# Optimization experiments

Measured on AMD Instinct MI355X. Metric: run time of the kernel, lower is better.

The kernel has to match this reference:

```python
import jax, jax.numpy as jnp
import numpy as np

T, N, E = 8, 50000, 800000
XD, HD, GD, ZD, TD, YHD = 128, 256, 128, 128, 8, 16
PSH = 100          # ps_predictor hidden width
BN_EPS = 1e-5


def _dense(k, fan_in, shape):
    return jax.random.normal(k, shape, jnp.float32) * (1.0 / np.sqrt(fan_in))


def setup_inputs() -> dict:
    ks = jax.random.split(jax.random.key(0), 20)
    inp = {}
    inp["X"] = jax.random.normal(ks[0], (T, N, XD), jnp.float32)
    inp["C"] = jax.random.uniform(ks[1], (T, N, TD), dtype=jnp.float32)
    inp["Y_hist"] = jax.random.normal(ks[2], (T, N, YHD), jnp.float32)
    inp["edge_index"] = jax.random.randint(ks[3], (T, 2, E), 0, N)
    # parameters
    inp["phi_W"] = _dense(ks[4], XD, (XD, HD)); inp["phi_b"] = jnp.zeros((HD,), jnp.float32)
    inp["gc_W"] = _dense(ks[5], HD, (T, HD, GD)); inp["gc_b"] = jnp.zeros((T, GD), jnp.float32)
    inp["ew_logit"] = jax.random.normal(ks[6], (T, E), jnp.float32) * 0.1  # learned edge weights (pre-sigmoid)
    inp["fuse_W"] = _dense(ks[7], 2 * HD + GD, (2 * HD + GD, ZD)); inp["fuse_b"] = jnp.zeros((ZD,), jnp.float32)
    inp["o00_W"] = _dense(ks[8], ZD, (ZD, ZD)); inp["o00_b"] = jnp.zeros((ZD,), jnp.float32)
    inp["o10_W"] = _dense(ks[9], ZD, (ZD, ZD)); inp["o10_b"] = jnp.zeros((ZD,), jnp.float32)
    inp["o01_W"] = _dense(ks[10], ZD, (ZD, 1)); inp["o01_b"] = jnp.zeros((1,), jnp.float32)
    inp["o11_W"] = _dense(ks[11], ZD, (ZD, 1)); inp["o11_b"] = jnp.zeros((1,), jnp.float32)
    inp["ps1_W"] = _dense(ks[12], ZD, (ZD, PSH)); inp["ps1_b"] = jnp.zeros((PSH,), jnp.float32)
    inp["bn_g"] = jnp.ones((PSH,), jnp.float32); inp["bn_b"] = jnp.zeros((PSH,), jnp.float32)
    inp["ps2_W"] = _dense(ks[13], PSH, (PSH, 2)); inp["ps2_b"] = jnp.zeros((2,), jnp.float32)
    inp["gru_Wih"] = _dense(ks[14], ZD + TD + YHD, (3 * HD, ZD + TD + YHD))
    inp["gru_Whh"] = _dense(ks[15], HD, (3 * HD, HD))
    inp["gru_bih"] = jnp.zeros((3 * HD,), jnp.float32)
    inp["gru_bhh"] = jnp.zeros((3 * HD,), jnp.float32)
    return inp


def reference(X, C, Y_hist, edge_index, phi_W, phi_b, gc_W, gc_b, ew_logit,
              fuse_W, fuse_b, o00_W, o00_b, o10_W, o10_b, o01_W, o01_b,
              o11_W, o11_b, ps1_W, ps1_b, bn_g, bn_b, ps2_W, ps2_b,
              gru_Wih, gru_Whh, gru_bih, gru_bhh):
    h0 = jnp.zeros((N, HD), X.dtype)
    bn_scale = bn_g / jnp.sqrt(1.0 + BN_EPS)  # eval-mode BN: running_mean=0, running_var=1

    def step(h, xs):
        x, ei, c, yh, W_t, b_t, ewl_t = xs
        phi = jax.nn.relu(x @ phi_W + phi_b)                              # [N,HD]
        # --- GCNConv with learned sigmoid edge weights + self loops ---
        src, dst = ei[0], ei[1]
        ew = jax.nn.sigmoid(ewl_t)                                        # [E]
        deg = jax.ops.segment_sum(ew, dst, num_segments=N) + 1.0          # +1 for self-loop weight
        dinv = jax.lax.rsqrt(deg)
        norm = dinv[src] * ew * dinv[dst]                                 # symmetric norm per edge
        xw = phi @ W_t                                                    # [N,GD]
        agg = jax.ops.segment_sum(norm[:, None] * xw[src], dst, num_segments=N)
        agg = agg + xw / deg[:, None] + b_t                               # self-loop contribution + bias
        rep = jax.nn.relu(agg)                                            # [N,GD] (dropout off in eval)
        # --- fuse with skip connection ---
        z = jax.nn.relu(jnp.concatenate([h, rep, phi], axis=1) @ fuse_W + fuse_b)  # [N,ZD]
        # --- GRUCell (torch gate order: reset, update, new) ---
        inp = jnp.concatenate([z, c, yh], axis=1)
        gi = inp @ gru_Wih.T + gru_bih
        gh = h @ gru_Whh.T + gru_bhh
        i_r, i_z, i_n = jnp.split(gi, 3, axis=1)
        h_r, h_z, h_n = jnp.split(gh, 3, axis=1)
        r = jax.nn.sigmoid(i_r + h_r)
        u = jax.nn.sigmoid(i_z + h_z)
        n = jnp.tanh(i_n + r * h_n)
        h_new = (1.0 - u) * n + u * h
        # --- outcome heads ---
        y0 = jax.nn.relu(z @ o00_W + o00_b) @ o01_W + o01_b               # [N,1]
        y1 = jax.nn.relu(z @ o10_W + o10_b) @ o11_W + o11_b               # [N,1]
        # --- propensity head (BatchNorm eval, sigmoid, softmax) ---
        s = jax.nn.sigmoid((z @ ps1_W + ps1_b) * bn_scale + bn_b)
        ps = jax.nn.softmax(s @ ps2_W + ps2_b, axis=1)                    # [N,2]
        return h_new, (y1, y0, z, ps)

    h_fin, (all_y1, all_y0, all_z, all_ps) = jax.lax.scan(
        step, h0, (X, edge_index, C, Y_hist, gc_W, gc_b, ew_logit))
    return all_y1, all_y0, all_z, all_ps, h_fin
```

## Files before the change

### kernel.cpp

```cpp
#include <hip/hip_runtime.h>
#include <math.h>

#define T_STEPS 8
#define NN 50000
#define EE 800000
#define TN (T_STEPS*NN)
#define TE (T_STEPS*EE)

typedef unsigned int uint;
typedef unsigned short ushort;
typedef unsigned long long u64;
typedef __attribute__((ext_vector_type(8))) short short8;
typedef __attribute__((ext_vector_type(4))) float f32x4;

__device__ __forceinline__ float sigf(float x){ return 1.0f/(1.0f+expf(-x)); }
__device__ __forceinline__ ushort f2b(float f){
  uint x = __float_as_uint(f);
  uint r = (x + 0x7fffu + ((x>>16)&1u)) >> 16;
  return (ushort)r;
}
__device__ __forceinline__ float b2f(ushort u){ return __uint_as_float(((uint)u)<<16); }

__device__ __forceinline__ void gload16(const ushort* g, ushort* l){
  __builtin_amdgcn_global_load_lds(
      (const __attribute__((address_space(1))) void*)g,
      (__attribute__((address_space(3))) void*)l, 16, 0, 0);
}

template<int ROWS>
__device__ __forceinline__ void stage_tile(const ushort* base, int ld, int rowclamp,
                                           ushort* lds, int lane, int wid){
  constexpr int ITERS = ROWS/32;
#pragma unroll
  for (int i=0;i<ITERS;i++){
    int lin = i*256 + wid*64 + lane;
    int row = lin>>3, s = lin&7;
    int gr = row; if (gr > rowclamp) gr = rowclamp;
    const ushort* gp = base + (size_t)gr*ld + ((s ^ (row&7))<<3);
    gload16(gp, lds + (size_t)(i*256 + wid*64)*8);
  }
}

__device__ __forceinline__ short8 fragld(const ushort* lds, int R, int kk, int lane){
  int slot = (kk*4 + (lane>>4)) ^ (R&7);
  return *(const short8*)&lds[R*64 + slot*8];
}

struct Seg { const ushort* p; int ld; long ts; int w; };

__global__ __launch_bounds__(256,2) void gemm_bf(
    Seg s0, Seg s1, Seg s2,
    const ushort* __restrict__ W, int K2, long Wts,
    const float* __restrict__ bias, int act,
    const ushort* __restrict__ addp, int ldad, long adts,
    float* __restrict__ C32, int ldc, long c32ts,
    ushort* __restrict__ C16, int ldb, long c16ts,
    int Nrow, int NOvalid)
{
  __shared__ __align__(16) ushort As[8192];
  __shared__ __align__(16) ushort Bs[8192];
  const int t    = blockIdx.z;
  const int tid  = threadIdx.x;
  const int lane = tid & 63;
  const int wid  = __builtin_amdgcn_readfirstlane(tid >> 6);
  const int brow = blockIdx.x*128;
  const int bcol = blockIdx.y*128;
  const int wr = wid>>1, wc = wid&1;

  f32x4 acc[4][4];
#pragma unroll
  for(int m=0;m<4;m++)
#pragma unroll
    for(int n=0;n<4;n++) acc[m][n] = (f32x4){0.f,0.f,0.f,0.f};

  const int nk = K2 >> 6;
  for (int kt=0; kt<nk; ++kt){
    int col0 = kt*64;
    const ushort* ab; int ald;
    if (col0 < s0.w){ ab = s0.p + (size_t)t*s0.ts + col0; ald = s0.ld; }
    else if (col0 < s0.w + s1.w){ ab = s1.p + (size_t)t*s1.ts + (col0 - s0.w); ald = s1.ld; }
    else { ab = s2.p + (size_t)t*s2.ts + (col0 - s0.w - s1.w); ald = s2.ld; }
    stage_tile<128>(ab + (size_t)brow*ald, ald, Nrow-1-brow, As, lane, wid);
    stage_tile<128>(W + (size_t)t*Wts + (size_t)bcol*K2 + col0, K2, 1<<30, Bs, lane, wid);
    __syncthreads();
#pragma unroll
    for (int kk=0;kk<2;kk++){
      short8 a[4], b[4];
#pragma unroll
      for (int m=0;m<4;m++) a[m] = fragld(As, wr*64 + m*16 + (lane&15), kk, lane);
#pragma unroll
      for (int n=0;n<4;n++) b[n] = fragld(Bs, wc*64 + n*16 + (lane&15), kk, lane);
#pragma unroll
      for (int m=0;m<4;m++)
#pragma unroll
        for (int n=0;n<4;n++)
          acc[m][n] = __builtin_amdgcn_mfma_f32_16x16x32_bf16(a[m], b[n], acc[m][n], 0,0,0);
    }
    __syncthreads();
  }
  const int rbase = brow + wr*64 + (lane>>4)*4;
  const int cbase = bcol + wc*64 + (lane&15);
#pragma unroll
  for (int m=0;m<4;m++){
#pragma unroll
    for (int q=0;q<4;q++){
      int r = rbase + m*16 + q;
      if (r >= Nrow) continue;
#pragma unroll
      for (int n=0;n<4;n++){
        int c = cbase + n*16;
        if (c >= NOvalid) continue;
        float v = acc[m][n][q];
        if (addp) v += b2f(addp[(size_t)t*adts + (size_t)r*ldad + c]);
        if (bias) v += bias[c];
        if (act==1) v = fmaxf(v, 0.f);
        if (C32) C32[(size_t)t*c32ts + (size_t)r*ldc + c] = v;
        if (C16) C16[(size_t)t*c16ts + (size_t)r*ldb + c] = f2b(v);
      }
    }
  }
}

__global__ __launch_bounds__(256,2) void gemm_gru(
    Seg s0, Seg s1, Seg s2,
    const ushort* __restrict__ W,
    const float* __restrict__ bg,
    const float* __restrict__ hin,
    float* __restrict__ hout, ushort* __restrict__ hbfo,
    int Nrow)
{
  __shared__ __align__(16) ushort As[8192];
  __shared__ __align__(16) ushort Bs[8192];
  const int tid  = threadIdx.x;
  const int lane = tid & 63;
  const int wid  = __builtin_amdgcn_readfirstlane(tid >> 6);
  const int brow = blockIdx.x*128;
  const int bcol = blockIdx.y*128;
  const int wr = wid>>1, wc = wid&1;
  const int K2 = 448;

  f32x4 acc[4][4];
#pragma unroll
  for(int m=0;m<4;m++)
#pragma unroll
    for(int n=0;n<4;n++) acc[m][n] = (f32x4){0.f,0.f,0.f,0.f};

  for (int kt=0; kt<7; ++kt){
    int col0 = kt*64;
    const ushort* ab; int ald;
    if (col0 < s0.w){ ab = s0.p + col0; ald = s0.ld; }
    else if (col0 < s0.w + s1.w){ ab = s1.p + (col0 - s0.w); ald = s1.ld; }
    else { ab = s2.p + (col0 - s0.w - s1.w); ald = s2.ld; }
    stage_tile<128>(ab + (size_t)brow*ald, ald, Nrow-1-brow, As, lane, wid);
    stage_tile<128>(W + (size_t)bcol*K2 + col0, K2, 1<<30, Bs, lane, wid);
    __syncthreads();
#pragma unroll
    for (int kk=0;kk<2;kk++){
      short8 a[4], b[4];
#pragma unroll
      for (int m=0;m<4;m++) a[m] = fragld(As, wr*64 + m*16 + (lane&15), kk, lane);
#pragma unroll
      for (int n=0;n<4;n++) b[n] = fragld(Bs, wc*64 + n*16 + (lane&15), kk, lane);
#pragma unroll
      for (int m=0;m<4;m++)
#pragma unroll
        for (int n=0;n<4;n++)
          acc[m][n] = __builtin_amdgcn_mfma_f32_16x16x32_bf16(a[m], b[n], acc[m][n], 0,0,0);
    }
    __syncthreads();
  }
  const int jj = lane&15;
  const int j  = blockIdx.y*32 + wc*16 + jj;
  const int rbase = brow + wr*64 + (lane>>4)*4;
  const int bcolw = bcol + wc*64;
  float bb[4];
#pragma unroll
  for (int n=0;n<4;n++) bb[n] = bg[bcolw + n*16 + jj];
#pragma unroll
  for (int m=0;m<4;m++){
#pragma unroll
    for (int q=0;q<4;q++){
      int r = rbase + m*16 + q;
      if (r >= Nrow) continue;
      float v0 = acc[m][0][q] + bb[0];
      float v1 = acc[m][1][q] + bb[1];
      float v2 = acc[m][2][q] + bb[2];
      float v3 = acc[m][3][q] + bb[3];
      float rg = sigf(v0), ug = sigf(v1);
      float ng = tanhf(v2 + rg*v3);
      float ho = hin[(size_t)r*256 + j];
      float hn = (1.f-ug)*ng + ug*ho;
      hout[(size_t)r*256 + j] = hn;
      hbfo[(size_t)r*256 + j] = f2b(hn);
    }
  }
}

__global__ __launch_bounds__(256,2) void heads_k(
    const ushort* __restrict__ Az, long Ats,
    const ushort* __restrict__ W,
    const float* __restrict__ o00b, const float* __restrict__ o10b,
    const float* __restrict__ w01, const float* __restrict__ b01,
    const float* __restrict__ w11, const float* __restrict__ b11,
    float* __restrict__ y0out, long y0ts,
    float* __restrict__ y1out, long y1ts, int Nrow)
{
  __shared__ __align__(16) ushort As[4096];
  __shared__ __align__(16) ushort Bs[16384];
  __shared__ float shy[4][64];
  const int t    = blockIdx.z;
  const int tid  = threadIdx.x;
  const int lane = tid & 63;
  const int wid  = __builtin_amdgcn_readfirstlane(tid >> 6);
  const int brow = blockIdx.x*64;
  const ushort* A = Az + (size_t)t*Ats;

  f32x4 acc[4][4];
#pragma unroll
  for(int m=0;m<4;m++)
#pragma unroll
    for(int n=0;n<4;n++) acc[m][n] = (f32x4){0.f,0.f,0.f,0.f};

  for (int kt=0; kt<2; ++kt){
    stage_tile<64>(A + (size_t)brow*128 + kt*64, 128, Nrow-1-brow, As, lane, wid);
    stage_tile<256>(W + kt*64, 128, 1<<30, Bs, lane, wid);
    __syncthreads();
#pragma unroll
    for (int kk=0;kk<2;kk++){
      short8 a[4], b[4];
#pragma unroll
      for (int m=0;m<4;m++) a[m] = fragld(As, m*16 + (lane&15), kk, lane);
#pragma unroll
      for (int n=0;n<4;n++) b[n] = fragld(Bs, wid*64 + n*16 + (lane&15), kk, lane);
#pragma unroll
      for (int m=0;m<4;m++)
#pragma unroll
        for (int n=0;n<4;n++)
          acc[m][n] = __builtin_amdgcn_mfma_f32_16x16x32_bf16(a[m], b[n], acc[m][n], 0,0,0);
    }
    __syncthreads();
  }
  float bb[4], ww[4];
#pragma unroll
  for (int n=0;n<4;n++){
    int c = wid*64 + n*16 + (lane&15);
    bb[n] = (c<128)? o00b[c] : o10b[c-128];
    ww[n] = (c<128)? w01[c]  : w11[c-128];
  }
#pragma unroll
  for (int m=0;m<4;m++){
#pragma unroll
    for (int q=0;q<4;q++){
      float p = 0.f;
#pragma unroll
      for (int n=0;n<4;n++) p += fmaxf(acc[m][n][q] + bb[n], 0.f) * ww[n];
#pragma unroll
      for (int o=1;o<16;o<<=1) p += __shfl_xor(p, o);
      if ((lane&15)==0) shy[wid][m*16 + (lane>>4)*4 + q] = p;
    }
  }
  __syncthreads();
  if (tid < 64){
    int r = brow + tid;
    if (r < Nrow){
      y0out[(size_t)t*y0ts + r] = shy[0][tid] + shy[1][tid] + b01[0];
      y1out[(size_t)t*y1ts + r] = shy[2][tid] + shy[3][tid] + b11[0];
    }
  }
}

__global__ __launch_bounds__(256,2) void ps_k(
    const ushort* __restrict__ Az, long Ats,
    const ushort* __restrict__ W,
    const float* __restrict__ psc, const float* __restrict__ psb,
    const float* __restrict__ W2, const float* __restrict__ b2,
    float* __restrict__ psout, long psts, int Nrow)
{
  __shared__ __align__(16) ushort As[8192];
  __shared__ __align__(16) ushort Bs[8192];
  __shared__ float sh0[2][128];
  __shared__ float sh1[2][128];
  const int t    = blockIdx.z;
  const int tid  = threadIdx.x;
  const int lane = tid & 63;
  const int wid  = __builtin_amdgcn_readfirstlane(tid >> 6);
  const int brow = blockIdx.x*128;
  const int wr = wid>>1, wc = wid&1;
  const ushort* A = Az + (size_t)t*Ats;

  f32x4 acc[4][4];
#pragma unroll
  for(int m=0;m<4;m++)
#pragma unroll
    for(int n=0;n<4;n++) acc[m][n] = (f32x4){0.f,0.f,0.f,0.f};

  for (int kt=0; kt<2; ++kt){
    stage_tile<128>(A + (size_t)brow*128 + kt*64, 128, Nrow-1-brow, As, lane, wid);
    stage_tile<128>(W + kt*64, 128, 1<<30, Bs, lane, wid);
    __syncthreads();
#pragma unroll
    for (int kk=0;kk<2;kk++){
      short8 a[4], b[4];
#pragma unroll
      for (int m=0;m<4;m++) a[m] = fragld(As, wr*64 + m*16 + (lane&15), kk, lane);
#pragma unroll
      for (int n=0;n<4;n++) b[n] = fragld(Bs, wc*64 + n*16 + (lane&15), kk, lane);
#pragma unroll
      for (int m=0;m<4;m++)
#pragma unroll
        for (int n=0;n<4;n++)
          acc[m][n] = __builtin_amdgcn_mfma_f32_16x16x32_bf16(a[m], b[n], acc[m][n], 0,0,0);
    }
    __syncthreads();
  }
  float sc[4], sb[4], w0_[4], w1_[4];
#pragma unroll
  for (int n=0;n<4;n++){
    int c = wc*64 + n*16 + (lane&15);
    bool ok = (c<100);
    sc[n] = ok? psc[c] : 0.f;
    sb[n] = ok? psb[c] : 0.f;
    w0_[n]= ok? W2[2*c] : 0.f;
    w1_[n]= ok? W2[2*c+1] : 0.f;
  }
#pragma unroll
  for (int m=0;m<4;m++){
#pragma unroll
    for (int q=0;q<4;q++){
      float a0=0.f, a1=0.f;
#pragma unroll
      for (int n=0;n<4;n++){
        float s = sigf(acc[m][n][q]*sc[n] + sb[n]);
        a0 += s*w0_[n]; a1 += s*w1_[n];
      }
#pragma unroll
      for (int o=1;o<16;o<<=1){ a0 += __shfl_xor(a0,o); a1 += __shfl_xor(a1,o); }
      if ((lane&15)==0){
        int rt = wr*64 + m*16 + (lane>>4)*4 + q;
        sh0[wc][rt] = a0; sh1[wc][rt] = a1;
      }
    }
  }
  __syncthreads();
  if (tid < 128){
    int r = brow + tid;
    if (r < Nrow){
      float l0 = sh0[0][tid]+sh0[1][tid]+b2[0];
      float l1 = sh1[0][tid]+sh1[1][tid]+b2[1];
      float mx = fmaxf(l0,l1);
      float e0 = expf(l0-mx), e1 = expf(l1-mx);
      float inv = 1.f/(e0+e1);
      psout[(size_t)t*psts + (size_t)r*2]   = e0*inv;
      psout[(size_t)t*psts + (size_t)r*2+1] = e1*inv;
    }
  }
}

__global__ void count_k(const int* __restrict__ ei, const float* __restrict__ ewl,
                        u64* __restrict__ degcnt)
{
  int idx = blockIdx.x*256 + threadIdx.x;
  if (idx >= TE) return;
  int t = idx / EE;
  int e = idx - t*EE;
  const int* dst = ei + (size_t)t*2*EE + EE;
  int d = dst[e];
  u64 v = (1ULL<<40) | (u64)(uint)(sigf(ewl[idx]) * 1048576.0f);
  atomicAdd((unsigned long long*)&degcnt[t*NN + d], (unsigned long long)v);
}

__global__ void dinv_k(const u64* __restrict__ degcnt, int* __restrict__ cnt,
                       float* __restrict__ dnv, float* __restrict__ invd){
  int idx = blockIdx.x*256+threadIdx.x;
  if (idx>=TN) return;
  u64 tot = degcnt[idx];
  int c = (int)(tot>>40);
  float S = (float)(tot & ((1ULL<<40)-1)) * (1.f/1048576.f);
  float dv = S + 1.f;
  cnt[idx] = c;
  dnv[idx]  = rsqrtf(dv);
  invd[idx] = 1.f/dv;
}

__global__ void scan1_k(const int* __restrict__ in, int* __restrict__ outv,
                        int* __restrict__ partials, int n)
{
  __shared__ int sh[256];
  int base = blockIdx.x*1024;
  int tid = threadIdx.x;
  int v[4]; int s=0;
#pragma unroll
  for (int i=0;i<4;i++){ int idx=base+tid*4+i; v[i] = (idx<n)? in[idx]:0; s+=v[i]; }
  sh[tid]=s; __syncthreads();
  for (int o=1;o<256;o<<=1){
    int t2 = (tid>=o)? sh[tid-o]:0;
    __syncthreads();
    sh[tid]+=t2;
    __syncthreads();
  }
  int excl = sh[tid]-s;
#pragma unroll
  for (int i=0;i<4;i++){ int idx=base+tid*4+i; if(idx<n) outv[idx]=excl; excl+=v[i]; }
  if (tid==255) partials[blockIdx.x]=sh[255];
}

__global__ void scan2_k(int* p, int np){
  __shared__ int sh[256];
  __shared__ int run;
  int tid=threadIdx.x;
  if(tid==0) run=0;
  __syncthreads();
  for(int base=0;base<np;base+=256){
    int v = (base+tid<np)? p[base+tid]:0;
    sh[tid]=v; __syncthreads();
    for(int o=1;o<256;o<<=1){
      int t2 = (tid>=o)? sh[tid-o]:0;
      __syncthreads();
      sh[tid]+=t2;
      __syncthreads();
    }
    int incl=sh[tid];
    int r0=run;
    __syncthreads();
    if(base+tid<np) p[base+tid]=r0+incl-v;
    __syncthreads();
    if(tid==0) run = r0 + sh[255];
    __syncthreads();
  }
}

__global__ void scan3_k(int* __restrict__ offs, const int* __restrict__ parts,
                        int* __restrict__ cur, int n){
  int idx = blockIdx.x*256+threadIdx.x;
  if (idx==0) offs[n] = TE;
  if (idx<n){ int v = offs[idx] + parts[idx>>10]; offs[idx]=v; cur[idx]=v; }
}

__global__ void fill_k(const int* __restrict__ ei, const float* __restrict__ ewl,
                       const float* __restrict__ dnv, int* __restrict__ cur,
                       uint* __restrict__ epack)
{
  int idx = blockIdx.x*256 + threadIdx.x;
  if (idx >= TE) return;
  int t = idx / EE;
  int e = idx - t*EE;
  const int* srcp = ei + (size_t)t*2*EE;
  const int* dstp = srcp + EE;
  int s=srcp[e], d=dstp[e];
  float nr = dnv[t*NN+s] * sigf(ewl[idx]) * dnv[t*NN+d];
  uint nq = (uint)(nr*65535.f + 0.5f);
  int pos = atomicAdd(&cur[t*NN+d], 1);
  epack[pos] = (uint)s | (nq<<16);
}

__global__ __launch_bounds__(256) void gather_k(const int* __restrict__ offs,
    const uint* __restrict__ epack,
    const ushort* __restrict__ xwb, const float* __restrict__ invd,
    const float* __restrict__ gcb, ushort* __restrict__ rep)
{
  int t    = blockIdx.z;
  int node = blockIdx.x*4 + (threadIdx.x>>6);
  int lane = threadIdx.x & 63;
  int half = lane>>5, ll = lane&31;
  if (node >= NN) return;
  const int* offs_t = offs + (size_t)t*NN;
  const ushort* xw_t = xwb + (size_t)t*NN*128;
  int o0 = offs_t[node], o1 = offs_t[node+1];
  float a0=0.f, a1=0.f, a2=0.f, a3=0.f;

  int j = o0 + half;
  for (; j+6 < o1; j += 8){
    uint e0 = epack[j],   e1 = epack[j+2];
    uint e2 = epack[j+4], e3 = epack[j+6];
    uint2 v0 = ((const uint2*)(xw_t + (size_t)(e0&0xffff)*128))[ll];
    uint2 v1 = ((const uint2*)(xw_t + (size_t)(e1&0xffff)*128))[ll];
    uint2 v2 = ((const uint2*)(xw_t + (size_t)(e2&0xffff)*128))[ll];
    uint2 v3 = ((const uint2*)(xw_t + (size_t)(e3&0xffff)*128))[ll];
    float n0 = (float)(e0>>16), n1 = (float)(e1>>16);
    float n2 = (float)(e2>>16), n3 = (float)(e3>>16);
    a0 = fmaf(n0, b2f((ushort)(v0.x&0xffff)), a0);
    a1 = fmaf(n0, b2f((ushort)(v0.x>>16)),   a1);
    a2 = fmaf(n0, b2f((ushort)(v0.y&0xffff)), a2);
    a3 = fmaf(n0, b2f((ushort)(v0.y>>16)),   a3);
    a0 = fmaf(n1, b2f((ushort)(v1.x&0xffff)), a0);
    a1 = fmaf(n1, b2f((ushort)(v1.x>>16)),   a1);
    a2 = fmaf(n1, b2f((ushort)(v1.y&0xffff)), a2);
    a3 = fmaf(n1, b2f((ushort)(v1.y>>16)),   a3);
    a0 = fmaf(n2, b2f((ushort)(v2.x&0xffff)), a0);
    a1 = fmaf(n2, b2f((ushort)(v2.x>>16)),   a1);
    a2 = fmaf(n2, b2f((ushort)(v2.y&0xffff)), a2);
    a3 = fmaf(n2, b2f((ushort)(v2.y>>16)),   a3);
    a0 = fmaf(n3, b2f((ushort)(v3.x&0xffff)), a0);
    a1 = fmaf(n3, b2f((ushort)(v3.x>>16)),   a1);
    a2 = fmaf(n3, b2f((ushort)(v3.y&0xffff)), a2);
    a3 = fmaf(n3, b2f((ushort)(v3.y>>16)),   a3);
  }
  for (; j < o1; j += 2){
    uint e0 = epack[j];
    uint2 v0 = ((const uint2*)(xw_t + (size_t)(e0&0xffff)*128))[ll];
    float n0 = (float)(e0>>16);
    a0 = fmaf(n0, b2f((ushort)(v0.x&0xffff)), a0);
    a1 = fmaf(n0, b2f((ushort)(v0.x>>16)),   a1);
    a2 = fmaf(n0, b2f((ushort)(v0.y&0xffff)), a2);
    a3 = fmaf(n0, b2f((ushort)(v0.y>>16)),   a3);
  }
  a0 += __shfl_xor(a0, 32);
  a1 += __shfl_xor(a1, 32);
  a2 += __shfl_xor(a2, 32);
  a3 += __shfl_xor(a3, 32);
  const float qs = 1.f/65535.f;
  a0 *= qs; a1 *= qs; a2 *= qs; a3 *= qs;
  float sl = invd[(size_t)t*NN + node];
  uint2 us = ((const uint2*)(xw_t + (size_t)node*128))[ll];
  float4 gb = ((const float4*)(gcb + (size_t)t*128))[ll];
  a0 = fmaf(sl, b2f((ushort)(us.x&0xffff)), a0) + gb.x;
  a1 = fmaf(sl, b2f((ushort)(us.x>>16)),   a1) + gb.y;
  a2 = fmaf(sl, b2f((ushort)(us.y&0xffff)), a2) + gb.z;
  a3 = fmaf(sl, b2f((ushort)(us.y>>16)),   a3) + gb.w;
  a0 = fmaxf(a0,0.f); a1 = fmaxf(a1,0.f);
  a2 = fmaxf(a2,0.f); a3 = fmaxf(a3,0.f);
  if (half==0){
    uint pk0 = (uint)f2b(a0) | ((uint)f2b(a1)<<16);
    uint pk1 = (uint)f2b(a2) | ((uint)f2b(a3)<<16);
    ((uint2*)(rep + ((size_t)t*NN + node)*128))[ll] = make_uint2(pk0, pk1);
  }
}

__global__ void convT_k(ushort* __restrict__ dst, const float* __restrict__ src,
                        int O, int Osrc, int K, int Kp)
{
  int idx = blockIdx.x*256 + threadIdx.x;
  if (idx >= O*Kp) return;
  dst += (size_t)blockIdx.y * O * Kp;
  src += (size_t)blockIdx.y * K * Osrc;
  int o = idx / Kp, k = idx - o*Kp;
  float v = (k<K && o<Osrc) ? src[(size_t)k*Osrc + o] : 0.f;
  dst[idx] = f2b(v);
}

__global__ void woc_k(ushort* __restrict__ dst, const float* __restrict__ o00W,
                      const float* __restrict__ o10W)
{
  int idx = blockIdx.x*256 + threadIdx.x;
  if (idx >= 256*128) return;
  int o = idx >> 7, k = idx & 127;
  float v = (o<128) ? o00W[(size_t)k*128 + o] : o10W[(size_t)k*128 + (o-128)];
  dst[idx] = f2b(v);
}

__global__ void wgru_k(const float* __restrict__ Wih, const float* __restrict__ Whh,
                       const float* __restrict__ bih, const float* __restrict__ bhh,
                       ushort* __restrict__ Wg, float* __restrict__ bg)
{
  int idx = blockIdx.x*256 + threadIdx.x;
  if (idx >= 1024*448) return;
  int c = idx/448, k = idx - c*448;
  int G = c>>6, g = (c>>4)&3, jj = c&15;
  int j = G*16 + jj;
  float v = 0.f;
  if (k < 152){
    if      (g==0) v = Wih[(size_t)j*152 + k];
    else if (g==1) v = Wih[(size_t)(256+j)*152 + k];
    else if (g==2) v = Wih[(size_t)(512+j)*152 + k];
  } else if (k >= 192){
    int kk = k-192;
    if      (g==0) v = Whh[(size_t)j*256 + kk];
    else if (g==1) v = Whh[(size_t)(256+j)*256 + kk];
    else if (g==3) v = Whh[(size_t)(512+j)*256 + kk];
  }
  Wg[idx] = f2b(v);
  if (k==0){
    float b;
    if      (g==0) b = bih[j]     + bhh[j];
    else if (g==1) b = bih[256+j] + bhh[256+j];
    else if (g==2) b = bih[512+j];
    else           b = bhh[512+j];
    bg[c] = b;
  }
}

__global__ void misc_k(const float* __restrict__ ps1b, const float* __restrict__ bng,
                       const float* __restrict__ bnb,
                       float* __restrict__ psc, float* __restrict__ psb)
{
  int i = threadIdx.x;
  if (i<100){ float sc = bng[i]*rsqrtf(1.f+1e-5f); psc[i]=sc; psb[i]=ps1b[i]*sc+bnb[i]; }
  else if (i<128){ psc[i]=0.f; psb[i]=0.f; }
}

__global__ void xconv_k(ushort* __restrict__ dst, const float* __restrict__ src, long n4)
{
  long i = (long)blockIdx.x*256 + threadIdx.x;
  if (i >= n4) return;
  float4 v = ((const float4*)src)[i];
  uint lo = (uint)f2b(v.x) | ((uint)f2b(v.y)<<16);
  uint hi = (uint)f2b(v.z) | ((uint)f2b(v.w)<<16);
  ((uint2*)dst)[i] = make_uint2(lo, hi);
}

__global__ void cyh_k(ushort* __restrict__ cyh, const float* __restrict__ Cc,
                      const float* __restrict__ Yh)
{
  long gid = (long)blockIdx.x*256 + threadIdx.x;
  if (gid >= (long)TN*64) return;
  long g = gid >> 6; int l = (int)(gid & 63);
  float v = 0.f;
  if (l < 8)       v = Cc[g*8 + l];
  else if (l < 24) v = Yh[g*16 + (l-8)];
  cyh[g*64 + l] = f2b(v);
}

extern "C" void kernel_launch(void* const* d_in, const int* in_sizes, int n_in,
                              void* d_out_v, int out_size, void* d_ws, size_t ws_size,
                              hipStream_t stream)
{
  const float* X    = (const float*)d_in[0];
  const float* Cc   = (const float*)d_in[1];
  const float* Yh   = (const float*)d_in[2];
  const int*   EI   = (const int*)  d_in[3];
  const float* phiW = (const float*)d_in[4];  const float* phib = (const float*)d_in[5];
  const float* gcW  = (const float*)d_in[6];  const float* gcb  = (const float*)d_in[7];
  const float* ewl  = (const float*)d_in[8];
  const float* fuseW= (const float*)d_in[9];  const float* fuseb= (const float*)d_in[10];
  const float* o00W = (const float*)d_in[11]; const float* o00b = (const float*)d_in[12];
  const float* o10W = (const float*)d_in[13]; const float* o10b = (const float*)d_in[14];
  const float* o01W = (const float*)d_in[15]; const float* o01b = (const float*)d_in[16];
  const float* o11W = (const float*)d_in[17]; const float* o11b = (const float*)d_in[18];
  const float* ps1W = (const float*)d_in[19]; const float* ps1b = (const float*)d_in[20];
  const float* bng  = (const float*)d_in[21]; const float* bnb  = (const float*)d_in[22];
  const float* ps2W = (const float*)d_in[23]; const float* ps2b = (const float*)d_in[24];
  const float* Wih  = (const float*)d_in[25]; const float* Whh  = (const float*)d_in[26];
  const float* bih  = (const float*)d_in[27]; const float* bhh  = (const float*)d_in[28];
  float* out = (float*)d_out_v;

  char* wsb = (char*)d_ws;
  size_t off=0;
  auto alloc=[&](size_t bytes)->void*{
    void* p = wsb + off;
    off = (off + bytes + 255) & ~(size_t)255;
    return p;
  };
  u64*   degcnt= (u64*)  alloc((size_t)TN*8);
  int*   cnt   = (int*)  alloc((size_t)TN*4);
  int*   cur   = (int*)  alloc((size_t)TN*4);
  int*   offs  = (int*)  alloc(((size_t)TN+1)*4);
  float* dnv   = (float*)alloc((size_t)TN*4);
  float* invd  = (float*)alloc((size_t)TN*4);
  uint*  epack = (uint*) alloc((size_t)TE*4);
  int*   parts = (int*)  alloc(4096);
  ushort* Xb   = (ushort*)alloc((size_t)TN*128*2);
  ushort* phiA = (ushort*)alloc((size_t)TN*256*2);
  ushort* xwb  = (ushort*)alloc((size_t)TN*128*2);
  ushort* pz   = (ushort*)alloc((size_t)TN*128*2);
  ushort* hbf0 = (ushort*)alloc((size_t)NN*256*2);
  ushort* hbf1 = (ushort*)alloc((size_t)NN*256*2);
  float*  hb   = (float*)alloc((size_t)NN*256*4);
  ushort* phiWt= (ushort*)alloc(256*128*2);
  ushort* gcWt = (ushort*)alloc((size_t)T_STEPS*128*256*2);
  ushort* WhT  = (ushort*)alloc(128*256*2);
  ushort* WrpT = (ushort*)alloc(128*384*2);
  ushort* Wgru = (ushort*)alloc((size_t)1024*448*2);
  float* bgru  = (float*)alloc(1024*4);
  ushort* wocT = (ushort*)alloc(256*128*2);
  ushort* ps1T = (ushort*)alloc(128*128*2);
  float* psc   = (float*)alloc(128*4);
  float* psb   = (float*)alloc(128*4);

  ushort* rep_all = Xb;
  ushort* zbf     = phiA;
  ushort* cyh     = phiA + (size_t)TN*128;

  hipMemsetAsync(degcnt, 0, (size_t)TN*8, stream);
  hipMemsetAsync(hb,   0, (size_t)NN*256*4, stream);
  hipMemsetAsync(hbf0, 0, (size_t)NN*256*2, stream);

  misc_k<<<1,256,0,stream>>>(ps1b,bng,bnb,psc,psb);
  convT_k<<<dim3((256*128+255)/256,1),256,0,stream>>>(phiWt, phiW, 256,256,128,128);
  convT_k<<<dim3((128*256+255)/256,T_STEPS),256,0,stream>>>(gcWt, gcW, 128,128,256,256);
  convT_k<<<dim3((128*256+255)/256,1),256,0,stream>>>(WhT, fuseW, 128,128,256,256);
  convT_k<<<dim3((128*384+255)/256,1),256,0,stream>>>(WrpT, fuseW+256*128, 128,128,384,384);
  convT_k<<<dim3((128*128+255)/256,1),256,0,stream>>>(ps1T, ps1W, 128,100,128,128);
  wgru_k<<<(1024*448+255)/256,256,0,stream>>>(Wih,Whh,bih,bhh,Wgru,bgru);
  woc_k<<<(256*128+255)/256,256,0,stream>>>(wocT, o00W, o10W);
  xconv_k<<<(int)(((size_t)TN*128/4+255)/256),256,0,stream>>>(Xb, X, (long)TN*128/4);

  count_k<<<(TE+255)/256,256,0,stream>>>(EI,ewl,degcnt);
  dinv_k<<<(TN+255)/256,256,0,stream>>>(degcnt,cnt,dnv,invd);
  scan1_k<<<(TN+1023)/1024,256,0,stream>>>(cnt,offs,parts,TN);
  scan2_k<<<1,256,0,stream>>>(parts,(TN+1023)/1024);
  scan3_k<<<(TN+255)/256,256,0,stream>>>(offs,parts,cur,TN);
  fill_k<<<(TE+255)/256,256,0,stream>>>(EI,ewl,dnv,cur,epack);

  const size_t zoff  = (size_t)2*TN;
  const size_t psoff = zoff + (size_t)TN*128;
  const size_t hoff  = psoff + (size_t)TN*2;
  constexpr int GX = (NN+127)/128;
  const Seg S0 = {nullptr,0,0,0};

  gemm_bf<<<dim3(GX,2,8),256,0,stream>>>(
    Seg{Xb,128,(long)NN*128,128}, S0, S0, phiWt,128,0, phib,1,
    nullptr,0,0, nullptr,0,0, phiA,256,(long)NN*256, NN,256);
  gemm_bf<<<dim3(GX,1,8),256,0,stream>>>(
    Seg{phiA,256,(long)NN*256,256}, S0, S0, gcWt,256,(long)128*256, nullptr,0,
    nullptr,0,0, nullptr,0,0, xwb,128,(long)NN*128, NN,128);
  gather_k<<<dim3(NN/4,1,8),256,0,stream>>>(offs, epack, xwb, invd, gcb, rep_all);
  gemm_bf<<<dim3(GX,1,8),256,0,stream>>>(
    Seg{rep_all,128,(long)NN*128,128}, Seg{phiA,256,(long)NN*256,256}, S0,
    WrpT,384,0, nullptr,0,
    nullptr,0,0, nullptr,0,0, pz,128,(long)NN*128, NN,128);
  cyh_k<<<(int)(((long)TN*64+255)/256),256,0,stream>>>(cyh, Cc, Yh);

  for (int t=0;t<T_STEPS;t++){
    const ushort* hbi = (t&1)? hbf1 : hbf0;
    ushort*       hbo = (t&1)? hbf0 : hbf1;
    float* hout = (t==T_STEPS-1)? (out+hoff) : hb;
    float* zt = out + zoff + (size_t)t*NN*128;
    ushort* zbt = zbf + (size_t)t*NN*128;
    gemm_bf<<<dim3(GX,1,1),256,0,stream>>>(
      Seg{hbi,256,0,256}, S0, S0, WhT,256,0, fuseb,1,
      pz + (size_t)t*NN*128,128,0, zt,128,0, zbt,128,0, NN,128);
    gemm_gru<<<dim3(GX,8),256,0,stream>>>(
      Seg{zbt,128,0,128}, Seg{cyh + (size_t)t*NN*64,64,0,64}, Seg{hbi,256,0,256},
      Wgru, bgru, hb, hout, hbo, NN);
  }

  heads_k<<<dim3((NN+63)/64,1,8),256,0,stream>>>(
    zbf,(long)NN*128, wocT, o00b,o10b, o01W,o01b, o11W,o11b,
    out + TN, (long)NN,
    out, (long)NN, NN);
  ps_k<<<dim3(GX,1,8),256,0,stream>>>(
    zbf,(long)NN*128, ps1T, psc,psb, ps2W,ps2b,
    out+psoff, (long)NN*2, NN);

  (void)in_sizes; (void)n_in; (void)out_size; (void)ws_size;
}
```

Baseline: 2.570 ms.

## Fuse X bf16 conversion into phi GEMM and widen GRU/phi tiles to 256 columns

```diff
diff --git a/kernel.cpp b/kernel.cpp
--- a/kernel.cpp
+++ b/kernel.cpp
@@ -121,7 +121,82 @@
   }
 }
 
-__global__ __launch_bounds__(256,2) void gemm_gru(
+__global__ __launch_bounds__(256,2) void gemm_phi256(
+    const float* __restrict__ A32, int ldA, long Ats,
+    const ushort* __restrict__ W, int K2,
+    const float* __restrict__ bias, int act,
+    ushort* __restrict__ C16, int ldb, long c16ts,
+    int Nrow)
+{
+  __shared__ __align__(16) ushort As[8192];
+  __shared__ __align__(16) ushort Bs[16384];
+  const int t    = blockIdx.z;
+  const int tid  = threadIdx.x;
+  const int lane = tid & 63;
+  const int wid  = __builtin_amdgcn_readfirstlane(tid >> 6);
+  const int brow = blockIdx.x*128;
+  const int wr = wid>>1, wc = wid&1;
+  const float* At = A32 + (size_t)t*Ats;
+
+  f32x4 acc[4][8];
+#pragma unroll
+  for(int m=0;m<4;m++)
+#pragma unroll
+    for(int n=0;n<8;n++) acc[m][n] = (f32x4){0.f,0.f,0.f,0.f};
+
+  const int nk = K2 >> 6;
+  for (int kt=0; kt<nk; ++kt){
+    int col0 = kt*64;
+#pragma unroll
+    for (int it=0; it<8; ++it){
+      int u = it*256 + tid;
+      int row = u >> 4;
+      int q4 = u & 15;
+      int grow = brow + row; if (grow >= Nrow) grow = Nrow-1;
+      float4 v = *(const float4*)&At[(size_t)grow*ldA + col0 + q4*4];
+      int s = q4 >> 1, half = q4 & 1;
+      uint lo = (uint)f2b(v.x) | ((uint)f2b(v.y)<<16);
+      uint hi = (uint)f2b(v.z) | ((uint)f2b(v.w)<<16);
+      *(uint2*)&As[row*64 + ((s ^ (row&7))<<3) + half*4] = make_uint2(lo,hi);
+    }
+    stage_tile<256>(W + col0, K2, 1<<30, Bs, lane, wid);
+    __syncthreads();
+#pragma unroll
+    for (int kk=0;kk<2;kk++){
+      short8 a[4], b[8];
+#pragma unroll
+      for (int m=0;m<4;m++) a[m] = fragld(As, wr*64 + m*16 + (lane&15), kk, lane);
+#pragma unroll
+      for (int n=0;n<8;n++) b[n] = fragld(Bs, wc*128 + n*16 + (lane&15), kk, lane);
+#pragma unroll
+      for (int m=0;m<4;m++)
+#pragma unroll
+        for (int n=0;n<8;n++)
+          acc[m][n] = __builtin_amdgcn_mfma_f32_16x16x32_bf16(a[m], b[n], acc[m][n], 0,0,0);
+    }
+    __syncthreads();
+  }
+  const int rbase = brow + wr*64 + (lane>>4)*4;
+  const int cbase = wc*128 + (lane&15);
+#pragma unroll
+  for (int m=0;m<4;m++){
+#pragma unroll
+    for (int q=0;q<4;q++){
+      int r = rbase + m*16 + q;
+      if (r >= Nrow) continue;
+#pragma unroll
+      for (int n=0;n<8;n++){
+        int c = cbase + n*16;
+        float v = acc[m][n][q];
+        if (bias) v += bias[c];
+        if (act==1) v = fmaxf(v, 0.f);
+        C16[(size_t)t*c16ts + (size_t)r*ldb + c] = f2b(v);
+      }
+    }
+  }
+}
+
+__global__ __launch_bounds__(256,2) void gemm_gru256(
     Seg s0, Seg s1, Seg s2,
     const ushort* __restrict__ W,
     const float* __restrict__ bg,
@@ -130,20 +205,20 @@
     int Nrow)
 {
   __shared__ __align__(16) ushort As[8192];
-  __shared__ __align__(16) ushort Bs[8192];
+  __shared__ __align__(16) ushort Bs[16384];
   const int tid  = threadIdx.x;
   const int lane = tid & 63;
   const int wid  = __builtin_amdgcn_readfirstlane(tid >> 6);
   const int brow = blockIdx.x*128;
-  const int bcol = blockIdx.y*128;
+  const int bcol = blockIdx.y*256;
   const int wr = wid>>1, wc = wid&1;
   const int K2 = 448;
 
-  f32x4 acc[4][4];
+  f32x4 acc[4][8];
 #pragma unroll
   for(int m=0;m<4;m++)
 #pragma unroll
-    for(int n=0;n<4;n++) acc[m][n] = (f32x4){0.f,0.f,0.f,0.f};
+    for(int n=0;n<8;n++) acc[m][n] = (f32x4){0.f,0.f,0.f,0.f};
 
   for (int kt=0; kt<7; ++kt){
     int col0 = kt*64;
@@ -152,46 +227,50 @@
     else if (col0 < s0.w + s1.w){ ab = s1.p + (col0 - s0.w); ald = s1.ld; }
     else { ab = s2.p + (col0 - s0.w - s1.w); ald = s2.ld; }
     stage_tile<128>(ab + (size_t)brow*ald, ald, Nrow-1-brow, As, lane, wid);
-    stage_tile<128>(W + (size_t)bcol*K2 + col0, K2, 1<<30, Bs, lane, wid);
+    stage_tile<256>(W + (size_t)bcol*K2 + col0, K2, 1<<30, Bs, lane, wid);
     __syncthreads();
 #pragma unroll
     for (int kk=0;kk<2;kk++){
-      short8 a[4], b[4];
+      short8 a[4], b[8];
 #pragma unroll
       for (int m=0;m<4;m++) a[m] = fragld(As, wr*64 + m*16 + (lane&15), kk, lane);
 #pragma unroll
-      for (int n=0;n<4;n++) b[n] = fragld(Bs, wc*64 + n*16 + (lane&15), kk, lane);
+      for (int n=0;n<8;n++) b[n] = fragld(Bs, wc*128 + n*16 + (lane&15), kk, lane);
 #pragma unroll
       for (int m=0;m<4;m++)
 #pragma unroll
-        for (int n=0;n<4;n++)
+        for (int n=0;n<8;n++)
           acc[m][n] = __builtin_amdgcn_mfma_f32_16x16x32_bf16(a[m], b[n], acc[m][n], 0,0,0);
     }
     __syncthreads();
   }
   const int jj = lane&15;
-  const int j  = blockIdx.y*32 + wc*16 + jj;
   const int rbase = brow + wr*64 + (lane>>4)*4;
-  const int bcolw = bcol + wc*64;
-  float bb[4];
-#pragma unroll
-  for (int n=0;n<4;n++) bb[n] = bg[bcolw + n*16 + jj];
-#pragma unroll
-  for (int m=0;m<4;m++){
-#pragma unroll
-    for (int q=0;q<4;q++){
-      int r = rbase + m*16 + q;
-      if (r >= Nrow) continue;
-      float v0 = acc[m][0][q] + bb[0];
-      float v1 = acc[m][1][q] + bb[1];
-      float v2 = acc[m][2][q] + bb[2];
-      float v3 = acc[m][3][q] + bb[3];
-      float rg = sigf(v0), ug = sigf(v1);
-      float ng = tanhf(v2 + rg*v3);
-      float ho = hin[(size_t)r*256 + j];
-      float hn = (1.f-ug)*ng + ug*ho;
-      hout[(size_t)r*256 + j] = hn;
-      hbfo[(size_t)r*256 + j] = f2b(hn);
+  const int Gbase = blockIdx.y*4 + wc*2;
+#pragma unroll
+  for (int ng=0; ng<2; ++ng){
+    const int G = Gbase + ng;
+    const int j = G*16 + jj;
+    float bb[4];
+#pragma unroll
+    for (int g=0;g<4;g++) bb[g] = bg[G*64 + g*16 + jj];
+#pragma unroll
+    for (int m=0;m<4;m++){
+#pragma unroll
+      for (int q=0;q<4;q++){
+        int r = rbase + m*16 + q;
+        if (r >= Nrow) continue;
+        float v0 = acc[m][ng*4+0][q] + bb[0];
+        float v1 = acc[m][ng*4+1][q] + bb[1];
+        float v2 = acc[m][ng*4+2][q] + bb[2];
+        float v3 = acc[m][ng*4+3][q] + bb[3];
+        float rg = sigf(v0), ug = sigf(v1);
+        float ngv = tanhf(v2 + rg*v3);
+        float ho = hin[(size_t)r*256 + j];
+        float hn = (1.f-ug)*ngv + ug*ho;
+        hout[(size_t)r*256 + j] = hn;
+        hbfo[(size_t)r*256 + j] = f2b(hn);
+      }
     }
   }
 }
@@ -450,7 +529,7 @@
   float nr = dnv[t*NN+s] * sigf(ewl[idx]) * dnv[t*NN+d];
   uint nq = (uint)(nr*65535.f + 0.5f);
   int pos = atomicAdd(&cur[t*NN+d], 1);
-  epack[pos] = (uint)s | (nq<<16);
+  __builtin_nontemporal_store((uint)s | (nq<<16), &epack[pos]);
 }
 
 __global__ __launch_bounds__(256) void gather_k(const int* __restrict__ offs,
@@ -458,8 +537,9 @@
     const ushort* __restrict__ xwb, const float* __restrict__ invd,
     const float* __restrict__ gcb, ushort* __restrict__ rep)
 {
-  int t    = blockIdx.z;
-  int node = blockIdx.x*4 + (threadIdx.x>>6);
+  int bid  = blockIdx.x;
+  int t    = bid & 7;
+  int node = (bid>>3)*4 + (threadIdx.x>>6);
   int lane = threadIdx.x & 63;
   int half = lane>>5, ll = lane&31;
   if (node >= NN) return;
@@ -588,16 +668,6 @@
   else if (i<128){ psc[i]=0.f; psb[i]=0.f; }
 }
 
-__global__ void xconv_k(ushort* __restrict__ dst, const float* __restrict__ src, long n4)
-{
-  long i = (long)blockIdx.x*256 + threadIdx.x;
-  if (i >= n4) return;
-  float4 v = ((const float4*)src)[i];
-  uint lo = (uint)f2b(v.x) | ((uint)f2b(v.y)<<16);
-  uint hi = (uint)f2b(v.z) | ((uint)f2b(v.w)<<16);
-  ((uint2*)dst)[i] = make_uint2(lo, hi);
-}
-
 __global__ void cyh_k(ushort* __restrict__ cyh, const float* __restrict__ Cc,
                       const float* __restrict__ Yh)
 {
@@ -648,7 +718,7 @@
   float* invd  = (float*)alloc((size_t)TN*4);
   uint*  epack = (uint*) alloc((size_t)TE*4);
   int*   parts = (int*)  alloc(4096);
-  ushort* Xb   = (ushort*)alloc((size_t)TN*128*2);
+  ushort* rep_all = (ushort*)alloc((size_t)TN*128*2);
   ushort* phiA = (ushort*)alloc((size_t)TN*256*2);
   ushort* xwb  = (ushort*)alloc((size_t)TN*128*2);
   ushort* pz   = (ushort*)alloc((size_t)TN*128*2);
@@ -666,7 +736,6 @@
   float* psc   = (float*)alloc(128*4);
   float* psb   = (float*)alloc(128*4);
 
-  ushort* rep_all = Xb;
   ushort* zbf     = phiA;
   ushort* cyh     = phiA + (size_t)TN*128;
 
@@ -682,7 +751,6 @@
   convT_k<<<dim3((128*128+255)/256,1),256,0,stream>>>(ps1T, ps1W, 128,100,128,128);
   wgru_k<<<(1024*448+255)/256,256,0,stream>>>(Wih,Whh,bih,bhh,Wgru,bgru);
   woc_k<<<(256*128+255)/256,256,0,stream>>>(wocT, o00W, o10W);
-  xconv_k<<<(int)(((size_t)TN*128/4+255)/256),256,0,stream>>>(Xb, X, (long)TN*128/4);
 
   count_k<<<(TE+255)/256,256,0,stream>>>(EI,ewl,degcnt);
   dinv_k<<<(TN+255)/256,256,0,stream>>>(degcnt,cnt,dnv,invd);
@@ -697,13 +765,12 @@
   constexpr int GX = (NN+127)/128;
   const Seg S0 = {nullptr,0,0,0};
 
-  gemm_bf<<<dim3(GX,2,8),256,0,stream>>>(
-    Seg{Xb,128,(long)NN*128,128}, S0, S0, phiWt,128,0, phib,1,
-    nullptr,0,0, nullptr,0,0, phiA,256,(long)NN*256, NN,256);
+  gemm_phi256<<<dim3(GX,1,8),256,0,stream>>>(
+    X,128,(long)NN*128, phiWt,128, phib,1, phiA,256,(long)NN*256, NN);
   gemm_bf<<<dim3(GX,1,8),256,0,stream>>>(
     Seg{phiA,256,(long)NN*256,256}, S0, S0, gcWt,256,(long)128*256, nullptr,0,
     nullptr,0,0, nullptr,0,0, xwb,128,(long)NN*128, NN,128);
-  gather_k<<<dim3(NN/4,1,8),256,0,stream>>>(offs, epack, xwb, invd, gcb, rep_all);
+  gather_k<<<(NN/4)*8,256,0,stream>>>(offs, epack, xwb, invd, gcb, rep_all);
   gemm_bf<<<dim3(GX,1,8),256,0,stream>>>(
     Seg{rep_all,128,(long)NN*128,128}, Seg{phiA,256,(long)NN*256,256}, S0,
     WrpT,384,0, nullptr,0,
@@ -719,7 +786,7 @@
     gemm_bf<<<dim3(GX,1,1),256,0,stream>>>(
       Seg{hbi,256,0,256}, S0, S0, WhT,256,0, fuseb,1,
       pz + (size_t)t*NN*128,128,0, zt,128,0, zbt,128,0, NN,128);
-    gemm_gru<<<dim3(GX,8),256,0,stream>>>(
+    gemm_gru256<<<dim3(GX,4),256,0,stream>>>(
       Seg{zbt,128,0,128}, Seg{cyh + (size_t)t*NN*64,64,0,64}, Seg{hbi,256,0,256},
       Wgru, bgru, hb, hout, hbo, NN);
   }
```

Result: slower. 2.773 ms (+7.9%).

## Widen GRU GEMM to 512-thread 128x256 tiles and replace CSR fill atomics with ranks

Applied to the files above, without the earlier changes.

```diff
diff --git a/kernel.cpp b/kernel.cpp
--- a/kernel.cpp
+++ b/kernel.cpp
@@ -38,6 +38,20 @@
     int gr = row; if (gr > rowclamp) gr = rowclamp;
     const ushort* gp = base + (size_t)gr*ld + ((s ^ (row&7))<<3);
     gload16(gp, lds + (size_t)(i*256 + wid*64)*8);
+  }
+}
+
+template<int ROWS>
+__device__ __forceinline__ void stage512(const ushort* base, int ld, int rowclamp,
+                                         ushort* lds, int tid){
+  constexpr int ITERS = ROWS/64;
+#pragma unroll
+  for (int i=0;i<ITERS;i++){
+    int lin = i*512 + tid;
+    int row = lin>>3, s = lin&7;
+    int gr = row; if (gr > rowclamp) gr = rowclamp;
+    const ushort* gp = base + (size_t)gr*ld + ((s ^ (row&7))<<3);
+    gload16(gp, lds + (size_t)lin*8);
   }
 }
 
@@ -121,7 +135,7 @@
   }
 }
 
-__global__ __launch_bounds__(256,2) void gemm_gru(
+__global__ __launch_bounds__(512,2) void gemm_gru512(
     Seg s0, Seg s1, Seg s2,
     const ushort* __restrict__ W,
     const float* __restrict__ bg,
@@ -130,13 +144,13 @@
     int Nrow)
 {
   __shared__ __align__(16) ushort As[8192];
-  __shared__ __align__(16) ushort Bs[8192];
+  __shared__ __align__(16) ushort Bs[16384];
   const int tid  = threadIdx.x;
   const int lane = tid & 63;
   const int wid  = __builtin_amdgcn_readfirstlane(tid >> 6);
   const int brow = blockIdx.x*128;
-  const int bcol = blockIdx.y*128;
-  const int wr = wid>>1, wc = wid&1;
+  const int bcol = blockIdx.y*256;
+  const int wr = wid>>2, wc = wid&3;
   const int K2 = 448;
 
   f32x4 acc[4][4];
@@ -151,8 +165,8 @@
     if (col0 < s0.w){ ab = s0.p + col0; ald = s0.ld; }
     else if (col0 < s0.w + s1.w){ ab = s1.p + (col0 - s0.w); ald = s1.ld; }
     else { ab = s2.p + (col0 - s0.w - s1.w); ald = s2.ld; }
-    stage_tile<128>(ab + (size_t)brow*ald, ald, Nrow-1-brow, As, lane, wid);
-    stage_tile<128>(W + (size_t)bcol*K2 + col0, K2, 1<<30, Bs, lane, wid);
+    stage512<128>(ab + (size_t)brow*ald, ald, Nrow-1-brow, As, tid);
+    stage512<256>(W + (size_t)bcol*K2 + col0, K2, 1<<30, Bs, tid);
     __syncthreads();
 #pragma unroll
     for (int kk=0;kk<2;kk++){
@@ -170,12 +184,12 @@
     __syncthreads();
   }
   const int jj = lane&15;
-  const int j  = blockIdx.y*32 + wc*16 + jj;
+  const int G  = blockIdx.y*4 + wc;
+  const int j  = G*16 + jj;
   const int rbase = brow + wr*64 + (lane>>4)*4;
-  const int bcolw = bcol + wc*64;
   float bb[4];
 #pragma unroll
-  for (int n=0;n<4;n++) bb[n] = bg[bcolw + n*16 + jj];
+  for (int n=0;n<4;n++) bb[n] = bg[G*64 + n*16 + jj];
 #pragma unroll
   for (int m=0;m<4;m++){
 #pragma unroll
@@ -357,7 +371,7 @@
 }
 
 __global__ void count_k(const int* __restrict__ ei, const float* __restrict__ ewl,
-                        u64* __restrict__ degcnt)
+                        u64* __restrict__ degcnt, ushort* __restrict__ rank)
 {
   int idx = blockIdx.x*256 + threadIdx.x;
   if (idx >= TE) return;
@@ -366,7 +380,8 @@
   const int* dst = ei + (size_t)t*2*EE + EE;
   int d = dst[e];
   u64 v = (1ULL<<40) | (u64)(uint)(sigf(ewl[idx]) * 1048576.0f);
-  atomicAdd((unsigned long long*)&degcnt[t*NN + d], (unsigned long long)v);
+  u64 old = atomicAdd((unsigned long long*)&degcnt[t*NN + d], (unsigned long long)v);
+  rank[idx] = (ushort)(old>>40);
 }
 
 __global__ void dinv_k(const u64* __restrict__ degcnt, int* __restrict__ cnt,
@@ -429,16 +444,15 @@
   }
 }
 
-__global__ void scan3_k(int* __restrict__ offs, const int* __restrict__ parts,
-                        int* __restrict__ cur, int n){
+__global__ void scan3_k(int* __restrict__ offs, const int* __restrict__ parts, int n){
   int idx = blockIdx.x*256+threadIdx.x;
   if (idx==0) offs[n] = TE;
-  if (idx<n){ int v = offs[idx] + parts[idx>>10]; offs[idx]=v; cur[idx]=v; }
+  if (idx<n){ offs[idx] = offs[idx] + parts[idx>>10]; }
 }
 
 __global__ void fill_k(const int* __restrict__ ei, const float* __restrict__ ewl,
-                       const float* __restrict__ dnv, int* __restrict__ cur,
-                       uint* __restrict__ epack)
+                       const float* __restrict__ dnv, const int* __restrict__ offs,
+                       const ushort* __restrict__ rank, uint* __restrict__ epack)
 {
   int idx = blockIdx.x*256 + threadIdx.x;
   if (idx >= TE) return;
@@ -449,7 +463,7 @@
   int s=srcp[e], d=dstp[e];
   float nr = dnv[t*NN+s] * sigf(ewl[idx]) * dnv[t*NN+d];
   uint nq = (uint)(nr*65535.f + 0.5f);
-  int pos = atomicAdd(&cur[t*NN+d], 1);
+  int pos = offs[t*NN+d] + rank[idx];
   epack[pos] = (uint)s | (nq<<16);
 }
 
@@ -642,11 +656,11 @@
   };
   u64*   degcnt= (u64*)  alloc((size_t)TN*8);
   int*   cnt   = (int*)  alloc((size_t)TN*4);
-  int*   cur   = (int*)  alloc((size_t)TN*4);
   int*   offs  = (int*)  alloc(((size_t)TN+1)*4);
   float* dnv   = (float*)alloc((size_t)TN*4);
   float* invd  = (float*)alloc((size_t)TN*4);
   uint*  epack = (uint*) alloc((size_t)TE*4);
+  ushort* rankb= (ushort*)alloc((size_t)TE*2);
   int*   parts = (int*)  alloc(4096);
   ushort* Xb   = (ushort*)alloc((size_t)TN*128*2);
   ushort* phiA = (ushort*)alloc((size_t)TN*256*2);
@@ -684,12 +698,12 @@
   woc_k<<<(256*128+255)/256,256,0,stream>>>(wocT, o00W, o10W);
   xconv_k<<<(int)(((size_t)TN*128/4+255)/256),256,0,stream>>>(Xb, X, (long)TN*128/4);
 
-  count_k<<<(TE+255)/256,256,0,stream>>>(EI,ewl,degcnt);
+  count_k<<<(TE+255)/256,256,0,stream>>>(EI,ewl,degcnt,rankb);
   dinv_k<<<(TN+255)/256,256,0,stream>>>(degcnt,cnt,dnv,invd);
   scan1_k<<<(TN+1023)/1024,256,0,stream>>>(cnt,offs,parts,TN);
   scan2_k<<<1,256,0,stream>>>(parts,(TN+1023)/1024);
-  scan3_k<<<(TN+255)/256,256,0,stream>>>(offs,parts,cur,TN);
-  fill_k<<<(TE+255)/256,256,0,stream>>>(EI,ewl,dnv,cur,epack);
+  scan3_k<<<(TN+255)/256,256,0,stream>>>(offs,parts,TN);
+  fill_k<<<(TE+255)/256,256,0,stream>>>(EI,ewl,dnv,offs,rankb,epack);
 
   const size_t zoff  = (size_t)2*TN;
   const size_t psoff = zoff + (size_t)TN*128;
@@ -719,7 +733,7 @@
     gemm_bf<<<dim3(GX,1,1),256,0,stream>>>(
       Seg{hbi,256,0,256}, S0, S0, WhT,256,0, fuseb,1,
       pz + (size_t)t*NN*128,128,0, zt,128,0, zbt,128,0, NN,128);
-    gemm_gru<<<dim3(GX,8),256,0,stream>>>(
+    gemm_gru512<<<dim3(GX,4),512,0,stream>>>(
       Seg{zbt,128,0,128}, Seg{cyh + (size_t)t*NN*64,64,0,64}, Seg{hbi,256,0,256},
       Wgru, bgru, hb, hout, hbo, NN);
   }
```

Result: faster. 2.404 ms (-6.5%).
